# Optimization experiments

Measured on AMD Instinct MI355X. Metric: run time of the kernel, lower is better.

Reference implementation:

```python
import jax, jax.numpy as jnp
import numpy as np

M_LCG = 65539
RAND_MAX = 4294967295
SEED = 123
LEVEL = 1e-9
BN_EPS = 0.8  # nn.BatchNorm1d(in_planes, 0.8) -> eps=0.8


def _pool_random_noise(seed, n):
    # Faithful Python reimplementation of Random + PoolRandom (deterministic
    # given seed and n, so it is a compile-time constant for jit).
    s = seed
    def irand():
        nonlocal s
        s = (M_LCG * s + 1) & RAND_MAX
        return s
    pool = [irand() for _ in range(n)]
    nxt = n - 1
    out = np.empty(n, dtype=np.float64)
    for i in range(n):
        nxt = pool[nxt] % n
        out[i] = pool[nxt]
        pool[nxt] = irand()
    return jnp.asarray(out * LEVEL, dtype=jnp.float32)


def setup_inputs() -> dict:
    key = jax.random.key(0)
    k_x, k_w = jax.random.split(key)
    B, C_in, C_out = 8192, 4096, 4096
    x = jax.random.normal(k_x, (B, C_in), dtype=jnp.float32)
    gamma = jnp.ones((C_in,), dtype=jnp.float32)
    beta = jnp.zeros((C_in,), dtype=jnp.float32)
    W = jax.random.normal(k_w, (C_out, C_in), dtype=jnp.float32) / np.sqrt(C_in)
    b = jnp.zeros((C_out,), dtype=jnp.float32)
    return {"x": x, "gamma": gamma, "beta": beta, "W": W, "b": b}


def reference(x, gamma, beta, W, b):
    C = x.shape[1]
    noise = _pool_random_noise(SEED, C)          # [C], constant
    h = jax.nn.relu(x + noise[None, :])          # noise-add + ReLU
    # BatchNorm1d (training mode): stats over batch per channel, biased var
    mean = jnp.mean(h, axis=0)
    var = jnp.mean(jnp.square(h - mean[None, :]), axis=0)
    hn = (h - mean[None, :]) * jax.lax.rsqrt(var + BN_EPS)
    hn = hn * gamma[None, :] + beta[None, :]
    # 1x1 Conv1d over length-1 sequence == linear layer
    z = jnp.einsum('bc,oc->bo', hn, W) + b[None, :]
    return z
```

## Files before the change

kernel.cpp:

```cpp
#include <hip/hip_runtime.h>


#define B_ROWS 8192
#define C_CH   4096
#define N_OUT  4096

struct alignas(16) NoiseTable { float v[C_CH]; };

constexpr NoiseTable make_noise() {
    unsigned s = 123u;
    unsigned pool[C_CH] = {};
    for (int i = 0; i < C_CH; ++i) { s = 65539u * s + 1u; pool[i] = s; }
    int nxt = C_CH - 1;
    NoiseTable t{};
    for (int i = 0; i < C_CH; ++i) {
        nxt = (int)(pool[nxt] % (unsigned)C_CH);
        t.v[i] = (float)((double)pool[nxt] * 1e-9);
        s = 65539u * s + 1u;
        pool[nxt] = s;
    }
    return t;
}

__device__ constexpr NoiseTable NOISE = make_noise();

__device__ __forceinline__ unsigned short f2bf(float f) {
    unsigned u = __builtin_bit_cast(unsigned, f);
    unsigned r = (u + 0x7FFFu + ((u >> 16) & 1u)) >> 16;
    return (unsigned short)r;
}

typedef __attribute__((ext_vector_type(8))) short bf16x8;
typedef __attribute__((ext_vector_type(4))) float f32x4;

__device__ __forceinline__ void gload16(const void* g, void* l) {
    __builtin_amdgcn_global_load_lds(
        (const __attribute__((address_space(1))) void*)g,
        (__attribute__((address_space(3))) void*)l, 16, 0, 0);
}

#define BARRIER()  do { __builtin_amdgcn_s_barrier(); asm volatile("" ::: "memory"); } while (0)
#define SCHED0()   __builtin_amdgcn_sched_barrier(0)
#define LGKM(N)    do { asm volatile("s_waitcnt lgkmcnt(" #N ")" ::: "memory"); \
                        __builtin_amdgcn_sched_barrier(0); } while (0)

__global__ __launch_bounds__(256) void conv_h_kernel(const float* __restrict__ x,
                                                     unsigned short* __restrict__ Hbf,
                                                     float* __restrict__ psum,
                                                     float* __restrict__ psumsq) {
    const int t = threadIdx.x;
    const int b = blockIdx.x;

    float4 nv[4];
    #pragma unroll
    for (int g = 0; g < 4; ++g)
        nv[g] = *reinterpret_cast<const float4*>(&NOISE.v[g * 1024 + 4 * t]);

    float4 s[4], q[4];
    #pragma unroll
    for (int g = 0; g < 4; ++g) { s[g] = make_float4(0,0,0,0); q[g] = make_float4(0,0,0,0); }

    const int row0 = b * 16;
    for (int r = 0; r < 16; ++r) {
        const size_t rb = (size_t)(row0 + r) * C_CH;
        const float* xr = x + rb;
        #pragma unroll
        for (int g = 0; g < 4; ++g) {
            float4 v = *reinterpret_cast<const float4*>(&xr[g * 1024 + 4 * t]);
            float h0 = fmaxf(v.x + nv[g].x, 0.f);
            float h1 = fmaxf(v.y + nv[g].y, 0.f);
            float h2 = fmaxf(v.z + nv[g].z, 0.f);
            float h3 = fmaxf(v.w + nv[g].w, 0.f);
            s[g].x += h0; s[g].y += h1; s[g].z += h2; s[g].w += h3;
            q[g].x += h0*h0; q[g].y += h1*h1; q[g].z += h2*h2; q[g].w += h3*h3;
            ushort4 o;
            o.x = f2bf(h0); o.y = f2bf(h1); o.z = f2bf(h2); o.w = f2bf(h3);
            *reinterpret_cast<ushort4*>(&Hbf[rb + g * 1024 + 4 * t]) = o;
        }
    }
    #pragma unroll
    for (int g = 0; g < 4; ++g) {
        *reinterpret_cast<float4*>(&psum  [(size_t)b * C_CH + g * 1024 + 4 * t]) = s[g];
        *reinterpret_cast<float4*>(&psumsq[(size_t)b * C_CH + g * 1024 + 4 * t]) = q[g];
    }
}

__global__ __launch_bounds__(256) void finalize_kernel(const float* __restrict__ psum,
                                                       const float* __restrict__ psumsq,
                                                       const float* __restrict__ gamma,
                                                       const float* __restrict__ beta,
                                                       float* __restrict__ scale,
                                                       float* __restrict__ shift) {
    __shared__ float ls[8][32], lq[8][32];
    const int t  = threadIdx.x;
    const int c  = blockIdx.x * 32 + (t & 31);
    const int g  = t >> 5;
    float s = 0.f, q = 0.f;
    const int bk0 = g * 64;
    for (int bk = bk0; bk < bk0 + 64; ++bk) {
        s += psum  [(size_t)bk * C_CH + c];
        q += psumsq[(size_t)bk * C_CH + c];
    }
    ls[g][t & 31] = s; lq[g][t & 31] = q;
    __syncthreads();
    if (t < 32) {
        float S = 0.f, Q = 0.f;
        #pragma unroll
        for (int g2 = 0; g2 < 8; ++g2) { S += ls[g2][t]; Q += lq[g2][t]; }
        const int ch = blockIdx.x * 32 + t;
        const float inv  = 1.f / (float)B_ROWS;
        const float mean = S * inv;
        const float var  = fmaxf(Q * inv - mean * mean, 0.f);
        const float sc   = gamma[ch] / sqrtf(var + 0.8f);
        scale[ch] = sc;
        shift[ch] = beta[ch] - mean * sc;
    }
}

__global__ __launch_bounds__(256) void convW_kernel(const float* __restrict__ W,
                                                    const float* __restrict__ scale,
                                                    const float* __restrict__ shift,
                                                    const float* __restrict__ b,
                                                    unsigned short* __restrict__ Wbf,
                                                    float* __restrict__ biasN) {
    const int wv   = threadIdx.x >> 6;
    const int lane = threadIdx.x & 63;
    const int o    = blockIdx.x * 4 + wv;
    const float* wr = W + (size_t)o * C_CH;
    unsigned short* wo = Wbf + (size_t)o * C_CH;

    float acc = 0.f;
    #pragma unroll
    for (int s = 0; s < 16; ++s) {
        const int c = s * 256 + lane * 4;
        float4 v  = *reinterpret_cast<const float4*>(&wr[c]);
        float4 sc = *reinterpret_cast<const float4*>(&scale[c]);
        float4 sh = *reinterpret_cast<const float4*>(&shift[c]);
        ushort4 ov;
        ov.x = f2bf(v.x * sc.x); ov.y = f2bf(v.y * sc.y);
        ov.z = f2bf(v.z * sc.z); ov.w = f2bf(v.w * sc.w);
        *reinterpret_cast<ushort4*>(&wo[c]) = ov;
        acc += sh.x * v.x + sh.y * v.y + sh.z * v.z + sh.w * v.w;
    }
    #pragma unroll
    for (int off = 32; off > 0; off >>= 1)
        acc += __shfl_down(acc, off);
    if (lane == 0) biasN[o] = b[o] + acc;
}


template<int MH, int NH>
__device__ __forceinline__ void quad_mfma(bf16x8 (&af)[4][2], bf16x8 (&bfr)[4][2],
                                          f32x4 (&acc)[8][4]) {
    #pragma unroll
    for (int s = 0; s < 2; ++s)
        #pragma unroll
        for (int m = 0; m < 4; ++m)
            #pragma unroll
            for (int n = 0; n < 2; ++n)
                acc[MH * 4 + m][NH * 2 + n] = __builtin_amdgcn_mfma_f32_16x16x32_bf16(
                    af[m][s], bfr[NH * 2 + n][s], acc[MH * 4 + m][NH * 2 + n], 0, 0, 0);
}

template<bool STG>
__device__ __forceinline__ void tile_step(
    char* lds, const int bc, const int bn,
    const char*& pA0, const char*& pA1, const char*& pA2, const char*& pA3,
    const char*& pB0, const char*& pB1, const char*& pB2, const char*& pB3,
    const int dstw, const int aoff0, const int aoff1,
    const int boff0, const int boff1,
    f32x4 (&acc)[8][4]) {

    bf16x8 af[4][2], bfr[4][2];

    asm volatile("s_waitcnt vmcnt(2)" ::: "memory");
    BARRIER();
    SCHED0();
    if (STG) {
        gload16(pB0, lds + bn + 32768 + dstw);
        gload16(pB1, lds + bn + 40960 + dstw);
    }
    #pragma unroll
    for (int m = 0; m < 4; ++m) {
        af[m][0] = *reinterpret_cast<const bf16x8*>(lds + bc + aoff0 + m * 2048);
        af[m][1] = *reinterpret_cast<const bf16x8*>(lds + bc + aoff1 + m * 2048);
    }
    #pragma unroll
    for (int n = 0; n < 2; ++n) {
        bfr[n][0] = *reinterpret_cast<const bf16x8*>(lds + bc + boff0 + n * 2048);
        bfr[n][1] = *reinterpret_cast<const bf16x8*>(lds + bc + boff1 + n * 2048);
    }
    SCHED0();
    #pragma unroll
    for (int n = 2; n < 4; ++n) {
        bfr[n][0] = *reinterpret_cast<const bf16x8*>(lds + bc + boff0 + n * 2048);
        bfr[n][1] = *reinterpret_cast<const bf16x8*>(lds + bc + boff1 + n * 2048);
    }
    LGKM(4);
    __builtin_amdgcn_s_setprio(1);
    quad_mfma<0, 0>(af, bfr, acc);
    __builtin_amdgcn_s_setprio(0);
    if (STG) {
        gload16(pB2, lds + bn + 49152 + dstw);
        gload16(pB3, lds + bn + 57344 + dstw);
    }
    LGKM(0);
    __builtin_amdgcn_s_setprio(1);
    quad_mfma<0, 1>(af, bfr, acc);
    __builtin_amdgcn_s_setprio(0);

    if (STG) asm volatile("s_waitcnt vmcnt(4)" ::: "memory");
    else     asm volatile("s_waitcnt vmcnt(0)" ::: "memory");
    BARRIER();
    SCHED0();
    if (STG) {
        gload16(pA0, lds + bn +     0 + dstw);
        gload16(pA2, lds + bn + 16384 + dstw);
    }
    #pragma unroll
    for (int m = 0; m < 2; ++m) {
        af[m][0] = *reinterpret_cast<const bf16x8*>(lds + bc + aoff0 + (m + 4) * 2048);
        af[m][1] = *reinterpret_cast<const bf16x8*>(lds + bc + aoff1 + (m + 4) * 2048);
    }
    SCHED0();
    #pragma unroll
    for (int m = 2; m < 4; ++m) {
        af[m][0] = *reinterpret_cast<const bf16x8*>(lds + bc + aoff0 + (m + 4) * 2048);
        af[m][1] = *reinterpret_cast<const bf16x8*>(lds + bc + aoff1 + (m + 4) * 2048);
    }
    LGKM(4);
    __builtin_amdgcn_s_setprio(1);
    #pragma unroll
    for (int s = 0; s < 2; ++s)
        #pragma unroll
        for (int m = 0; m < 2; ++m)
            #pragma unroll
            for (int n = 2; n < 4; ++n)
                acc[4 + m][n] = __builtin_amdgcn_mfma_f32_16x16x32_bf16(
                    af[m][s], bfr[n][s], acc[4 + m][n], 0, 0, 0);
    __builtin_amdgcn_s_setprio(0);
    if (STG) {
        gload16(pA1, lds + bn +  8192 + dstw);
        gload16(pA3, lds + bn + 24576 + dstw);
        pA0 += 128; pA1 += 128; pA2 += 128; pA3 += 128;
        pB0 += 128; pB1 += 128; pB2 += 128; pB3 += 128;
    }
    LGKM(0);
    __builtin_amdgcn_s_setprio(1);
    #pragma unroll
    for (int s = 0; s < 2; ++s)
        #pragma unroll
        for (int m = 2; m < 4; ++m)
            #pragma unroll
            for (int n = 2; n < 4; ++n)
                acc[4 + m][n] = __builtin_amdgcn_mfma_f32_16x16x32_bf16(
                    af[m][s], bfr[n][s], acc[4 + m][n], 0, 0, 0);
    #pragma unroll
    for (int s = 0; s < 2; ++s)
        #pragma unroll
        for (int m = 0; m < 4; ++m)
            #pragma unroll
            for (int n = 0; n < 2; ++n)
                acc[4 + m][n] = __builtin_amdgcn_mfma_f32_16x16x32_bf16(
                    af[m][s], bfr[n][s], acc[4 + m][n], 0, 0, 0);
    __builtin_amdgcn_s_setprio(0);
}

__global__ __launch_bounds__(512, 2) void gemm256_kernel(
    const unsigned short* __restrict__ A, const unsigned short* __restrict__ B,
    const float* __restrict__ bias, float* __restrict__ C) {
    constexpr int K = C_CH, N = N_OUT;
    __shared__ alignas(128) char lds[131072];

    const int nwg = gridDim.x;
    const int cpx = nwg >> 3;
    int wg = blockIdx.x;
    wg = (wg & 7) * cpx + (wg >> 3);
    const int nbx = N >> 8;
    const int bx = wg % nbx, by = wg / nbx;
    const int row0 = by << 8, col0 = bx << 8;

    const int t    = threadIdx.x;
    const int lane = t & 63;
    const int wid  = t >> 6;
    const int wm   = wid >> 2;
    const int wn   = wid & 3;
    const int l15  = lane & 15;
    const int lh   = lane >> 4;

    const int sslot = (lane & 7) ^ (lane >> 3);
    const int dstw  = wid << 10;

    const char* pA0 = (const char*)A +
        ((size_t)(row0 + wid * 8 + (lane >> 3)) * K) * 2 + sslot * 16;
    const char* pA1 = pA0 + 1 * 64 * K * 2;
    const char* pA2 = pA0 + 2 * 64 * K * 2;
    const char* pA3 = pA0 + 3 * 64 * K * 2;
    const char* pB0 = (const char*)B +
        ((size_t)(col0 + wid * 8 + (lane >> 3)) * K) * 2 + sslot * 16;
    const char* pB1 = pB0 + 1 * 64 * K * 2;
    const char* pB2 = pB0 + 2 * 64 * K * 2;
    const char* pB3 = pB0 + 3 * 64 * K * 2;

    const int x7 = l15 & 7;
    const int aoff0 = wm * 16384 + l15 * 128 + ((lh     ) ^ x7) * 16;
    const int aoff1 = wm * 16384 + l15 * 128 + ((lh +  4) ^ x7) * 16;
    const int boff0 = 32768 + wn * 8192 + l15 * 128 + ((lh    ) ^ x7) * 16;
    const int boff1 = 32768 + wn * 8192 + l15 * 128 + ((lh + 4) ^ x7) * 16;

    f32x4 acc[8][4];
    #pragma unroll
    for (int m = 0; m < 8; ++m)
        #pragma unroll
        for (int n = 0; n < 4; ++n)
            acc[m][n] = (f32x4){0.f, 0.f, 0.f, 0.f};

    gload16(pB0, lds + 32768 + dstw);
    gload16(pB1, lds + 40960 + dstw);
    gload16(pB2, lds + 49152 + dstw);
    gload16(pB3, lds + 57344 + dstw);
    gload16(pA0, lds +     0 + dstw);
    gload16(pA2, lds + 16384 + dstw);
    gload16(pA1, lds +  8192 + dstw);
    gload16(pA3, lds + 24576 + dstw);
    pA0 += 128; pA1 += 128; pA2 += 128; pA3 += 128;
    pB0 += 128; pB1 += 128; pB2 += 128; pB3 += 128;

    #pragma unroll 1
    for (int it = 0; it < 31; ++it) {
        tile_step<true >(lds,     0, 65536, pA0, pA1, pA2, pA3, pB0, pB1, pB2, pB3,
                         dstw, aoff0, aoff1, boff0, boff1, acc);
        tile_step<true >(lds, 65536,     0, pA0, pA1, pA2, pA3, pB0, pB1, pB2, pB3,
                         dstw, aoff0, aoff1, boff0, boff1, acc);
    }
    tile_step<true >(lds,     0, 65536, pA0, pA1, pA2, pA3, pB0, pB1, pB2, pB3,
                     dstw, aoff0, aoff1, boff0, boff1, acc);
    tile_step<false>(lds, 65536,     0, pA0, pA1, pA2, pA3, pB0, pB1, pB2, pB3,
                     dstw, aoff0, aoff1, boff0, boff1, acc);

    const int crow0 = row0 + wm * 128 + lh * 4;
    const int ccol0 = col0 + wn * 64 + l15;
    #pragma unroll
    for (int n = 0; n < 4; ++n) {
        const float bv = bias[ccol0 + n * 16];
        #pragma unroll
        for (int m = 0; m < 8; ++m) {
            const size_t base = (size_t)(crow0 + m * 16) * N + (ccol0 + n * 16);
            #pragma unroll
            for (int j = 0; j < 4; ++j)
                C[base + (size_t)j * N] = acc[m][n][j] + bv;
        }
    }
}

extern "C" void kernel_launch(void* const* d_in, const int* in_sizes, int n_in,
                              void* d_out, int out_size, void* d_ws, size_t ws_size,
                              hipStream_t stream) {
    const float* x     = (const float*)d_in[0];
    const float* gamma = (const float*)d_in[1];
    const float* beta  = (const float*)d_in[2];
    const float* W     = (const float*)d_in[3];
    const float* b     = (const float*)d_in[4];
    float* out = (float*)d_out;

    char* ws = (char*)d_ws;
    unsigned short* Hbf = (unsigned short*)(ws);
    unsigned short* Wbf = (unsigned short*)(ws + 67108864);
    float* psum   = (float*)(ws + 100663296);
    float* psumsq = (float*)(ws + 109051904);
    float* scale  = (float*)(ws + 117440512);
    float* shift  = (float*)(ws + 117440512 + 16384);
    float* biasN  = (float*)(ws + 117440512 + 32768);

    hipLaunchKernelGGL(conv_h_kernel,   dim3(512),  dim3(256), 0, stream,
                       x, Hbf, psum, psumsq);
    hipLaunchKernelGGL(finalize_kernel, dim3(128),  dim3(256), 0, stream,
                       psum, psumsq, gamma, beta, scale, shift);
    hipLaunchKernelGGL(convW_kernel,    dim3(1024), dim3(256), 0, stream,
                       W, scale, shift, b, Wbf, biasN);
    hipLaunchKernelGGL(gemm256_kernel,  dim3(512),  dim3(512), 0, stream,
                       Hbf, Wbf, biasN, out);
}
```

Before: 292.0 us.

## Restructure GEMM pipeline to four-stage K=32 buffering with simpler swizzle

The main loop changes from double-buffered K=64 stages to four K=32 stages in the same 128KB of LDS. Three stages are prefetched up front, and each half-step issues loads for a stage further ahead. The LDS swizzle and the global load addressing are simplified to one pointer per operand with 64-byte rows. The aim is deeper latency hiding with more barriers per unit of K, but each barrier interval holds half as many MFMAs, so the added sync overhead could cancel the gain. It also drops the split lgkmcnt waits in favour of full waits.

```diff
diff --git a/kernel.cpp b/kernel.cpp
--- a/kernel.cpp
+++ b/kernel.cpp
@@ -41,7 +41,7 @@
 
 #define BARRIER()  do { __builtin_amdgcn_s_barrier(); asm volatile("" ::: "memory"); } while (0)
 #define SCHED0()   __builtin_amdgcn_sched_barrier(0)
-#define LGKM(N)    do { asm volatile("s_waitcnt lgkmcnt(" #N ")" ::: "memory"); \
+#define LGKM0()    do { asm volatile("s_waitcnt lgkmcnt(0)" ::: "memory"); \
                         __builtin_amdgcn_sched_barrier(0); } while (0)
 
 __global__ __launch_bounds__(256) void conv_h_kernel(const float* __restrict__ x,
@@ -149,120 +149,94 @@
 }
 
 
-template<int MH, int NH>
-__device__ __forceinline__ void quad_mfma(bf16x8 (&af)[4][2], bf16x8 (&bfr)[4][2],
-                                          f32x4 (&acc)[8][4]) {
-    #pragma unroll
-    for (int s = 0; s < 2; ++s)
-        #pragma unroll
-        for (int m = 0; m < 4; ++m)
-            #pragma unroll
-            for (int n = 0; n < 2; ++n)
-                acc[MH * 4 + m][NH * 2 + n] = __builtin_amdgcn_mfma_f32_16x16x32_bf16(
-                    af[m][s], bfr[NH * 2 + n][s], acc[MH * 4 + m][NH * 2 + n], 0, 0, 0);
-}
-
-template<bool STG>
+template<int MODE>
 __device__ __forceinline__ void tile_step(
-    char* lds, const int bc, const int bn,
-    const char*& pA0, const char*& pA1, const char*& pA2, const char*& pA3,
-    const char*& pB0, const char*& pB1, const char*& pB2, const char*& pB3,
-    const int dstw, const int aoff0, const int aoff1,
-    const int boff0, const int boff1,
-    f32x4 (&acc)[8][4]) {
-
-    bf16x8 af[4][2], bfr[4][2];
-
-    asm volatile("s_waitcnt vmcnt(2)" ::: "memory");
+    char* lds, const int rs0, const int rs1, const int ws0, const int ws1,
+    const char*& pA, const char*& pB, const int dstw,
+    const int aoff, const int boff, f32x4 (&acc)[8][4]) {
+
+    bf16x8 af[4], bfr[4];
+
+    if constexpr (MODE == 2) { asm volatile("s_waitcnt vmcnt(4)" ::: "memory"); }
+    else                     { asm volatile("s_waitcnt vmcnt(8)" ::: "memory"); }
     BARRIER();
     SCHED0();
-    if (STG) {
-        gload16(pB0, lds + bn + 32768 + dstw);
-        gload16(pB1, lds + bn + 40960 + dstw);
-    }
-    #pragma unroll
-    for (int m = 0; m < 4; ++m) {
-        af[m][0] = *reinterpret_cast<const bf16x8*>(lds + bc + aoff0 + m * 2048);
-        af[m][1] = *reinterpret_cast<const bf16x8*>(lds + bc + aoff1 + m * 2048);
-    }
-    #pragma unroll
-    for (int n = 0; n < 2; ++n) {
-        bfr[n][0] = *reinterpret_cast<const bf16x8*>(lds + bc + boff0 + n * 2048);
-        bfr[n][1] = *reinterpret_cast<const bf16x8*>(lds + bc + boff1 + n * 2048);
-    }
-    SCHED0();
-    #pragma unroll
-    for (int n = 2; n < 4; ++n) {
-        bfr[n][0] = *reinterpret_cast<const bf16x8*>(lds + bc + boff0 + n * 2048);
-        bfr[n][1] = *reinterpret_cast<const bf16x8*>(lds + bc + boff1 + n * 2048);
-    }
-    LGKM(4);
+    if constexpr (MODE <= 1) {
+        gload16(pA,           lds + ws0 +        dstw);
+        gload16(pA + 1048576, lds + ws0 + 8192 + dstw);
+        pA += 64;
+    }
+    #pragma unroll
+    for (int m = 0; m < 4; ++m)
+        af[m] = *reinterpret_cast<const bf16x8*>(lds + rs0 + aoff + m * 1024);
+    #pragma unroll
+    for (int n = 0; n < 4; ++n)
+        bfr[n] = *reinterpret_cast<const bf16x8*>(lds + rs0 + boff + n * 1024);
+    LGKM0();
     __builtin_amdgcn_s_setprio(1);
-    quad_mfma<0, 0>(af, bfr, acc);
+    #pragma unroll
+    for (int m = 0; m < 4; ++m)
+        #pragma unroll
+        for (int n = 0; n < 4; ++n)
+            acc[m][n] = __builtin_amdgcn_mfma_f32_16x16x32_bf16(af[m], bfr[n], acc[m][n], 0, 0, 0);
     __builtin_amdgcn_s_setprio(0);
-    if (STG) {
-        gload16(pB2, lds + bn + 49152 + dstw);
-        gload16(pB3, lds + bn + 57344 + dstw);
-    }
-    LGKM(0);
+
+    if constexpr (MODE <= 1) {
+        gload16(pB,           lds + ws0 + 16384 + dstw);
+        gload16(pB + 1048576, lds + ws0 + 24576 + dstw);
+        pB += 64;
+    }
+    #pragma unroll
+    for (int m = 0; m < 4; ++m)
+        af[m] = *reinterpret_cast<const bf16x8*>(lds + rs0 + aoff + (m + 4) * 1024);
+    LGKM0();
     __builtin_amdgcn_s_setprio(1);
-    quad_mfma<0, 1>(af, bfr, acc);
+    #pragma unroll
+    for (int m = 0; m < 4; ++m)
+        #pragma unroll
+        for (int n = 0; n < 4; ++n)
+            acc[4 + m][n] = __builtin_amdgcn_mfma_f32_16x16x32_bf16(af[m], bfr[n], acc[4 + m][n], 0, 0, 0);
     __builtin_amdgcn_s_setprio(0);
 
-    if (STG) asm volatile("s_waitcnt vmcnt(4)" ::: "memory");
-    else     asm volatile("s_waitcnt vmcnt(0)" ::: "memory");
+    if constexpr (MODE == 2) { asm volatile("s_waitcnt vmcnt(0)" ::: "memory"); }
+    else                     { asm volatile("s_waitcnt vmcnt(8)" ::: "memory"); }
     BARRIER();
     SCHED0();
-    if (STG) {
-        gload16(pA0, lds + bn +     0 + dstw);
-        gload16(pA2, lds + bn + 16384 + dstw);
-    }
-    #pragma unroll
-    for (int m = 0; m < 2; ++m) {
-        af[m][0] = *reinterpret_cast<const bf16x8*>(lds + bc + aoff0 + (m + 4) * 2048);
-        af[m][1] = *reinterpret_cast<const bf16x8*>(lds + bc + aoff1 + (m + 4) * 2048);
-    }
-    SCHED0();
-    #pragma unroll
-    for (int m = 2; m < 4; ++m) {
-        af[m][0] = *reinterpret_cast<const bf16x8*>(lds + bc + aoff0 + (m + 4) * 2048);
-        af[m][1] = *reinterpret_cast<const bf16x8*>(lds + bc + aoff1 + (m + 4) * 2048);
-    }
-    LGKM(4);
+    if constexpr (MODE == 0) {
+        gload16(pA,           lds + ws1 +        dstw);
+        gload16(pA + 1048576, lds + ws1 + 8192 + dstw);
+        pA += 64;
+    }
+    #pragma unroll
+    for (int m = 0; m < 4; ++m)
+        af[m] = *reinterpret_cast<const bf16x8*>(lds + rs1 + aoff + m * 1024);
+    #pragma unroll
+    for (int n = 0; n < 4; ++n)
+        bfr[n] = *reinterpret_cast<const bf16x8*>(lds + rs1 + boff + n * 1024);
+    LGKM0();
     __builtin_amdgcn_s_setprio(1);
     #pragma unroll
-    for (int s = 0; s < 2; ++s)
-        #pragma unroll
-        for (int m = 0; m < 2; ++m)
-            #pragma unroll
-            for (int n = 2; n < 4; ++n)
-                acc[4 + m][n] = __builtin_amdgcn_mfma_f32_16x16x32_bf16(
-                    af[m][s], bfr[n][s], acc[4 + m][n], 0, 0, 0);
+    for (int m = 0; m < 4; ++m)
+        #pragma unroll
+        for (int n = 0; n < 4; ++n)
+            acc[m][n] = __builtin_amdgcn_mfma_f32_16x16x32_bf16(af[m], bfr[n], acc[m][n], 0, 0, 0);
     __builtin_amdgcn_s_setprio(0);
-    if (STG) {
-        gload16(pA1, lds + bn +  8192 + dstw);
-        gload16(pA3, lds + bn + 24576 + dstw);
-        pA0 += 128; pA1 += 128; pA2 += 128; pA3 += 128;
-        pB0 += 128; pB1 += 128; pB2 += 128; pB3 += 128;
-    }
-    LGKM(0);
+
+    if constexpr (MODE == 0) {
+        gload16(pB,           lds + ws1 + 16384 + dstw);
+        gload16(pB + 1048576, lds + ws1 + 24576 + dstw);
+        pB += 64;
+    }
+    #pragma unroll
+    for (int m = 0; m < 4; ++m)
+        af[m] = *reinterpret_cast<const bf16x8*>(lds + rs1 + aoff + (m + 4) * 1024);
+    LGKM0();
     __builtin_amdgcn_s_setprio(1);
     #pragma unroll
-    for (int s = 0; s < 2; ++s)
-        #pragma unroll
-        for (int m = 2; m < 4; ++m)
-            #pragma unroll
-            for (int n = 2; n < 4; ++n)
-                acc[4 + m][n] = __builtin_amdgcn_mfma_f32_16x16x32_bf16(
-                    af[m][s], bfr[n][s], acc[4 + m][n], 0, 0, 0);
-    #pragma unroll
-    for (int s = 0; s < 2; ++s)
-        #pragma unroll
-        for (int m = 0; m < 4; ++m)
-            #pragma unroll
-            for (int n = 0; n < 2; ++n)
-                acc[4 + m][n] = __builtin_amdgcn_mfma_f32_16x16x32_bf16(
-                    af[m][s], bfr[n][s], acc[4 + m][n], 0, 0, 0);
+    for (int m = 0; m < 4; ++m)
+        #pragma unroll
+        for (int n = 0; n < 4; ++n)
+            acc[4 + m][n] = __builtin_amdgcn_mfma_f32_16x16x32_bf16(af[m], bfr[n], acc[4 + m][n], 0, 0, 0);
     __builtin_amdgcn_s_setprio(0);
 }
 
@@ -288,25 +262,15 @@
     const int l15  = lane & 15;
     const int lh   = lane >> 4;
 
-    const int sslot = (lane & 7) ^ (lane >> 3);
-    const int dstw  = wid << 10;
-
-    const char* pA0 = (const char*)A +
-        ((size_t)(row0 + wid * 8 + (lane >> 3)) * K) * 2 + sslot * 16;
-    const char* pA1 = pA0 + 1 * 64 * K * 2;
-    const char* pA2 = pA0 + 2 * 64 * K * 2;
-    const char* pA3 = pA0 + 3 * 64 * K * 2;
-    const char* pB0 = (const char*)B +
-        ((size_t)(col0 + wid * 8 + (lane >> 3)) * K) * 2 + sslot * 16;
-    const char* pB1 = pB0 + 1 * 64 * K * 2;
-    const char* pB2 = pB0 + 2 * 64 * K * 2;
-    const char* pB3 = pB0 + 3 * 64 * K * 2;
-
-    const int x7 = l15 & 7;
-    const int aoff0 = wm * 16384 + l15 * 128 + ((lh     ) ^ x7) * 16;
-    const int aoff1 = wm * 16384 + l15 * 128 + ((lh +  4) ^ x7) * 16;
-    const int boff0 = 32768 + wn * 8192 + l15 * 128 + ((lh    ) ^ x7) * 16;
-    const int boff1 = 32768 + wn * 8192 + l15 * 128 + ((lh + 4) ^ x7) * 16;
+    const int dstw = wid << 10;
+
+    const int sslot16 = (((t & 3) ^ ((t >> 3) & 3)) << 4);
+    const char* pA = (const char*)A + ((size_t)(row0 + (t >> 2)) * K) * 2 + sslot16;
+    const char* pB = (const char*)B + ((size_t)(col0 + (t >> 2)) * K) * 2 + sslot16;
+
+    const int axor16 = ((lh ^ ((l15 >> 1) & 3)) << 4);
+    const int aoff = ((wm << 7) + l15) * 64 + axor16;
+    const int boff = 16384 + ((wn << 6) + l15) * 64 + axor16;
 
     f32x4 acc[8][4];
     #pragma unroll
@@ -315,28 +279,32 @@
         for (int n = 0; n < 4; ++n)
             acc[m][n] = (f32x4){0.f, 0.f, 0.f, 0.f};
 
-    gload16(pB0, lds + 32768 + dstw);
-    gload16(pB1, lds + 40960 + dstw);
-    gload16(pB2, lds + 49152 + dstw);
-    gload16(pB3, lds + 57344 + dstw);
-    gload16(pA0, lds +     0 + dstw);
-    gload16(pA2, lds + 16384 + dstw);
-    gload16(pA1, lds +  8192 + dstw);
-    gload16(pA3, lds + 24576 + dstw);
-    pA0 += 128; pA1 += 128; pA2 += 128; pA3 += 128;
-    pB0 += 128; pB1 += 128; pB2 += 128; pB3 += 128;
+    gload16(pA,           lds +     0 + dstw);
+    gload16(pA + 1048576, lds +  8192 + dstw);
+    pA += 64;
+    gload16(pB,           lds + 16384 + dstw);
+    gload16(pB + 1048576, lds + 24576 + dstw);
+    pB += 64;
+    gload16(pA,           lds + 32768 +         dstw);
+    gload16(pA + 1048576, lds + 32768 +  8192 + dstw);
+    pA += 64;
+    gload16(pB,           lds + 32768 + 16384 + dstw);
+    gload16(pB + 1048576, lds + 32768 + 24576 + dstw);
+    pB += 64;
+    gload16(pA,           lds + 65536 +         dstw);
+    gload16(pA + 1048576, lds + 65536 +  8192 + dstw);
+    pA += 64;
+    gload16(pB,           lds + 65536 + 16384 + dstw);
+    gload16(pB + 1048576, lds + 65536 + 24576 + dstw);
+    pB += 64;
 
     #pragma unroll 1
     for (int it = 0; it < 31; ++it) {
-        tile_step<true >(lds,     0, 65536, pA0, pA1, pA2, pA3, pB0, pB1, pB2, pB3,
-                         dstw, aoff0, aoff1, boff0, boff1, acc);
-        tile_step<true >(lds, 65536,     0, pA0, pA1, pA2, pA3, pB0, pB1, pB2, pB3,
-                         dstw, aoff0, aoff1, boff0, boff1, acc);
-    }
-    tile_step<true >(lds,     0, 65536, pA0, pA1, pA2, pA3, pB0, pB1, pB2, pB3,
-                     dstw, aoff0, aoff1, boff0, boff1, acc);
-    tile_step<false>(lds, 65536,     0, pA0, pA1, pA2, pA3, pB0, pB1, pB2, pB3,
-                     dstw, aoff0, aoff1, boff0, boff1, acc);
+        tile_step<0>(lds,     0, 32768, 98304,     0, pA, pB, dstw, aoff, boff, acc);
+        tile_step<0>(lds, 65536, 98304, 32768, 65536, pA, pB, dstw, aoff, boff, acc);
+    }
+    tile_step<1>(lds,     0, 32768, 98304,     0, pA, pB, dstw, aoff, boff, acc);
+    tile_step<2>(lds, 65536, 98304, 32768, 65536, pA, pB, dstw, aoff, boff, acc);
 
     const int crow0 = row0 + wm * 128 + lh * 4;
     const int ccol0 = col0 + wn * 64 + l15;
```

Result: slower. 308.7 us (+5.7%).
